# Optimization experiments

Measured on AMD Instinct MI355X. Metric: run time of the kernel, lower is better.

The kernel has to match this reference:

```python
import jax, jax.numpy as jnp
import numpy as np
from jax import lax

DT = 0.01        # self.dt
DT_SCALE = 1.0   # forward default


def _christoffel(v, x, U, W):
    # Low-rank quadratic Christoffel contraction (U, W as in verlet_fused):
    # gamma = (tanh(x @ U) * (v @ U)^2) @ W        [B, D]
    h = v @ U                 # [B, R]
    gate = jnp.tanh(x @ U)    # [B, R]
    return (gate * h * h) @ W


def setup_inputs() -> dict:
    key = jax.random.key(0)
    ks = jax.random.split(key, 5)
    B, D, R = 4096, 1024, 256
    x = jax.random.normal(ks[0], (B, D), dtype=jnp.float32)
    v = jax.random.normal(ks[1], (B, D), dtype=jnp.float32)
    force = jax.random.normal(ks[2], (B, D), dtype=jnp.float32)
    U = jax.random.normal(ks[3], (D, R), dtype=jnp.float32) * (D ** -0.5)
    W = jax.random.normal(ks[4], (R, D), dtype=jnp.float32) * (R ** -0.5)
    return {"x": x, "v": v, "force": force, "U": U, "W": W, "steps": 8}


def reference(x, v, force, U, W, steps):
    dt = jnp.float32(DT * DT_SCALE)
    half = jnp.float32(0.5)

    def step(carry, _):
        x, v = carry
        a = force - _christoffel(v, x, U, W)
        v_half = v + half * dt * a
        x = x + dt * v_half
        a_next = force - _christoffel(v_half, x, U, W)
        v = v_half + half * dt * a_next
        return (x, v), None

    (x, v), _ = lax.scan(step, (x, v), None, length=steps)
    return (x, v)
```

## Files before the change

### kernel.cpp

```cpp
#include <hip/hip_runtime.h>

typedef __bf16 bf16_t;
typedef __bf16 bf16x2 __attribute__((ext_vector_type(2)));
typedef __bf16 bf16x8 __attribute__((ext_vector_type(8)));
typedef float f32x4 __attribute__((ext_vector_type(4)));

#define MFMA_BF16(a, b, c) __builtin_amdgcn_mfma_f32_16x16x32_bf16((a), (b), (c), 0, 0, 0)

static constexpr int Bn = 4096;
static constexpr int Dn = 1024;
static constexpr int Rn = 256;
static constexpr int BT = 16;
static constexpr float DTv = 0.01f;
static constexpr float HDT = 0.005f;

__device__ __forceinline__ int swz(int col) { return col ^ (((col >> 5) & 7) << 2); }

__global__ __launch_bounds__(1024)
void setup_kernel(const float* __restrict__ U, const float* __restrict__ W,
                  bf16_t* __restrict__ Upk, bf16_t* __restrict__ Wpk,
                  bf16_t* __restrict__ WUpk) {
  __shared__ __align__(16) bf16_t wbuf[16 * 1032];
  const int tid = (int)threadIdx.x;
  const int b = (int)blockIdx.x;
  if (b < 32) {
    int t = b * 1024 + tid;
    int l = t & 63, f = t >> 6;
    int kb = f & 31, ct = f >> 5;
    int row0 = kb * 32 + (l >> 4) * 8, col = ct * 16 + (l & 15);
    bf16x8 v;
#pragma unroll
    for (int j = 0; j < 8; ++j) v[j] = (bf16_t)U[(size_t)(row0 + j) * Rn + col];
    ((bf16x8*)Upk)[t] = v;
  } else if (b < 64) {
    int t = (b - 32) * 1024 + tid;
    int l = t & 63, f = t >> 6;
    int kb = f & 7, ct = f >> 3;
    int row0 = kb * 32 + (l >> 4) * 8, col = ct * 16 + (l & 15);
    bf16x8 v;
#pragma unroll
    for (int j = 0; j < 8; ++j) v[j] = (bf16_t)W[(size_t)(row0 + j) * Dn + col];
    ((bf16x8*)Wpk)[t] = v;
  } else {
    const int m = b - 64;
    const int wv = tid >> 6;
    const int l = tid & 63;
    const int ln = l & 15;
    const int quad = l >> 4;
    {
      int row = tid >> 6;
      int c0 = (tid & 63) * 16;
      const float* src = W + (size_t)(m * 16 + row) * Dn + c0;
      bf16_t* dst = wbuf + row * 1032 + c0;
#pragma unroll
      for (int j = 0; j < 16; ++j) dst[j] = (bf16_t)src[j];
    }
    __syncthreads();
    const int ucol = wv * 16 + ln;
    float uf[8][8];
#pragma unroll
    for (int p = 0; p < 8; ++p)
#pragma unroll
      for (int j = 0; j < 8; ++j)
        uf[p][j] = U[(size_t)(p * 32 + quad * 8 + j) * Rn + ucol];
    f32x4 acc = {0.f, 0.f, 0.f, 0.f};
    const bf16_t* arow = wbuf + ln * 1032 + quad * 8;
#pragma unroll
    for (int kb = 0; kb < 32; ++kb) {
      bf16x8 bb;
#pragma unroll
      for (int j = 0; j < 8; ++j) bb[j] = (bf16_t)uf[kb & 7][j];
      const bf16x8 a = *(const bf16x8*)(arow + kb * 32);
      acc = MFMA_BF16(a, bb, acc);
      if (kb < 24) {
#pragma unroll
        for (int j = 0; j < 8; ++j)
          uf[kb & 7][j] = U[(size_t)((kb + 8) * 32 + quad * 8 + j) * Rn + ucol];
      }
    }
#pragma unroll
    for (int r = 0; r < 4; ++r) {
      int rw = m * 16 + quad * 4 + r;
      int kb = rw >> 5;
      int sub = (rw >> 3) & 3;
      int j = rw & 7;
      size_t slot = ((size_t)(wv * 8 + kb) * 64 + sub * 16 + ln) * 8 + j;
      WUpk[slot] = (bf16_t)acc[r];
    }
  }
}

__global__ __launch_bounds__(1024)
__attribute__((amdgpu_waves_per_eu(4, 4)))
void integrate_kernel(const float* __restrict__ x_in, const float* __restrict__ v_in,
                      const float* __restrict__ force,
                      const bf16_t* __restrict__ Upk, const bf16_t* __restrict__ Wpk,
                      const bf16_t* __restrict__ WUpk,
                      const int* __restrict__ steps_p, float* __restrict__ out) {
  __shared__ __align__(16) char smem[99072];
  bf16_t* abuf = (bf16_t*)smem;
  float* fsb = (float*)smem;

  const int tid = (int)threadIdx.x;
  const int wv = tid >> 6;
  const int l = tid & 63;
  const int ln = l & 15;
  const int quad = l >> 4;
  const int s = steps_p[0];
  const int nhalf = 2 * s;
  const int row_base = (int)blockIdx.x * BT;

  float* out_x = out;
  float* out_v = out + (size_t)Bn * Dn;

  float xs[4][4], vs[4][4];
  bf16x2 fs2[4][2];

#pragma unroll
  for (int i = 0; i < 4; ++i) {
    const int col = (wv * 4 + i) * 16 + ln;
#pragma unroll
    for (int r = 0; r < 4; ++r) {
      const size_t g = (size_t)(row_base + quad * 4 + r) * Dn + col;
      xs[i][r] = x_in[g];
      vs[i][r] = v_in[g];
      fs2[i][r >> 1][r & 1] = (bf16_t)force[g];
    }
  }
#pragma unroll
  for (int i = 0; i < 4; ++i) {
    const int col = (wv * 4 + i) * 16 + ln;
#pragma unroll
    for (int r = 0; r < 4; ++r) {
      const int ro = (quad * 4 + r) * 1032 + col;
      abuf[ro] = (bf16_t)xs[i][r];
      abuf[16512 + ro] = (bf16_t)vs[i][r];
      abuf[33024 + ro] = fs2[i][r >> 1][r & 1];
    }
  }
  __syncthreads();

  f32x4 hx = {0.f, 0.f, 0.f, 0.f};
  f32x4 hv = {0.f, 0.f, 0.f, 0.f};
  f32x4 FU = {0.f, 0.f, 0.f, 0.f};
  {
    const bf16x8* up = (const bf16x8*)Upk + (size_t)wv * 32 * 64 + l;
    const bf16_t* ax = abuf + ln * 1032 + quad * 8;
    bf16x8 ur[8];
#pragma unroll
    for (int p = 0; p < 8; ++p) ur[p] = up[p * 64];
#pragma unroll
    for (int kb = 0; kb < 32; ++kb) {
      const bf16x8 b = ur[kb & 7];
      if (kb < 24) ur[kb & 7] = up[(kb + 8) * 64];
      const bf16x8 a0 = *(const bf16x8*)(ax + kb * 32);
      const bf16x8 a1 = *(const bf16x8*)(ax + 16512 + kb * 32);
      const bf16x8 a2 = *(const bf16x8*)(ax + 33024 + kb * 32);
      hx = MFMA_BF16(a0, b, hx);
      hv = MFMA_BF16(a1, b, hv);
      FU = MFMA_BF16(a2, b, FU);
    }
  }
  __syncthreads();

  bf16x8 wu[8];
  {
    const bf16x8* wub = (const bf16x8*)WUpk + (size_t)wv * 8 * 64 + l;
#pragma unroll
    for (int kb = 0; kb < 8; ++kb) wu[kb] = wub[kb * 64];
  }

  f32x4 S1 = {0.f, 0.f, 0.f, 0.f};
  f32x4 S2 = {0.f, 0.f, 0.f, 0.f};
  bf16_t* tbase = (bf16_t*)smem;
  for (int h = 0; h < nhalf; ++h) {
    if (h & 1) {
#pragma unroll
      for (int r = 0; r < 4; ++r) hx[r] += DTv * hv[r];
    }
    const float ch = (float)(s - ((h + 1) >> 1));
    bf16_t* tb = tbase + (h & 1) * 4224;
#pragma unroll
    for (int r = 0; r < 4; ++r) {
      float a = fminf(fmaxf(hx[r], -15.f), 15.f);
      const float e = __expf(2.f * a);
      const float gate = 1.f - 2.f * __builtin_amdgcn_rcpf(e + 1.f);
      const float t = gate * hv[r] * hv[r];
      S1[r] += t;
      S2[r] += ch * t;
      tb[(quad * 4 + r) * 264 + wv * 16 + ln] = (bf16_t)t;
    }
    __syncthreads();
    f32x4 g0 = {0.f, 0.f, 0.f, 0.f};
    f32x4 g1 = {0.f, 0.f, 0.f, 0.f};
    f32x4 g2 = {0.f, 0.f, 0.f, 0.f};
    f32x4 g3 = {0.f, 0.f, 0.f, 0.f};
    const bf16_t* trow = tb + ln * 264 + quad * 8;
    g0 = MFMA_BF16(*(const bf16x8*)(trow + 0 * 32), wu[0], g0);
    g1 = MFMA_BF16(*(const bf16x8*)(trow + 1 * 32), wu[1], g1);
    g2 = MFMA_BF16(*(const bf16x8*)(trow + 2 * 32), wu[2], g2);
    g3 = MFMA_BF16(*(const bf16x8*)(trow + 3 * 32), wu[3], g3);
    g0 = MFMA_BF16(*(const bf16x8*)(trow + 4 * 32), wu[4], g0);
    g1 = MFMA_BF16(*(const bf16x8*)(trow + 5 * 32), wu[5], g1);
    g2 = MFMA_BF16(*(const bf16x8*)(trow + 6 * 32), wu[6], g2);
    g3 = MFMA_BF16(*(const bf16x8*)(trow + 7 * 32), wu[7], g3);
#pragma unroll
    for (int r = 0; r < 4; ++r)
      hv[r] += HDT * (FU[r] - ((g0[r] + g1[r]) + (g2[r] + g3[r])));
  }
  __syncthreads();

  bf16_t* sbuf = (bf16_t*)smem;
#pragma unroll
  for (int r = 0; r < 4; ++r) {
    const int ro = (quad * 4 + r) * 264 + wv * 16 + ln;
    sbuf[ro] = (bf16_t)S1[r];
    sbuf[4224 + ro] = (bf16_t)S2[r];
  }
  __syncthreads();
  f32x4 ac1[4], ac2[4];
#pragma unroll
  for (int i = 0; i < 4; ++i) {
    ac1[i] = (f32x4){0.f, 0.f, 0.f, 0.f};
    ac2[i] = (f32x4){0.f, 0.f, 0.f, 0.f};
  }
  {
    const bf16x8* wp = (const bf16x8*)Wpk + (size_t)(wv * 4) * 8 * 64 + l;
    const bf16_t* s1row = sbuf + ln * 264 + quad * 8;
    const bf16_t* s2row = s1row + 4224;
    bf16x8 wr[4][2];
#pragma unroll
    for (int i = 0; i < 4; ++i) {
      wr[i][0] = wp[i * 512];
      wr[i][1] = wp[i * 512 + 64];
    }
#pragma unroll
    for (int kb = 0; kb < 8; ++kb) {
      const bf16x8 a1 = *(const bf16x8*)(s1row + kb * 32);
      const bf16x8 a2 = *(const bf16x8*)(s2row + kb * 32);
#pragma unroll
      for (int i = 0; i < 4; ++i) {
        const bf16x8 b = wr[i][kb & 1];
        if (kb < 6) wr[i][kb & 1] = wp[i * 512 + (kb + 2) * 64];
        ac1[i] = MFMA_BF16(a1, b, ac1[i]);
        ac2[i] = MFMA_BF16(a2, b, ac2[i]);
      }
    }
  }
  __syncthreads();

  const float sf = (float)s;
  const float c_vf = sf * DTv;
  const float c_xf = sf * sf * DTv * HDT;
  int csw[4];
#pragma unroll
  for (int i = 0; i < 4; ++i) csw[i] = swz((wv * 4 + i) * 16 + ln);
  auto store_chunk = [&](float* __restrict__ dstA, int HF, auto vex) {
    if ((quad >> 1) == HF) {
#pragma unroll
      for (int i = 0; i < 4; ++i)
#pragma unroll
        for (int r = 0; r < 4; ++r)
          fsb[((quad & 1) * 4 + r) * 1024 + csw[i]] = vex(i, r);
    }
    __syncthreads();
    float* dst_ = dstA + (size_t)(row_base + HF * 8) * Dn;
#pragma unroll
    for (int k = 0; k < 2; ++k) {
      const int fi = k * 4096 + tid * 4;
      *(f32x4*)(dst_ + fi) = *(const f32x4*)(fsb + (fi >> 10) * 1024 + swz(fi & 1023));
    }
    __syncthreads();
  };
  auto vval = [&](int i, int r) {
    return vs[i][r] + c_vf * (float)fs2[i][r >> 1][r & 1] - HDT * ac1[i][r];
  };
  auto xval = [&](int i, int r) {
    return xs[i][r] + c_vf * vs[i][r] + c_xf * (float)fs2[i][r >> 1][r & 1] -
           DTv * HDT * ac2[i][r];
  };
  store_chunk(out_v, 0, vval);
  store_chunk(out_v, 1, vval);
  store_chunk(out_x, 0, xval);
  store_chunk(out_x, 1, xval);
}

extern "C" void kernel_launch(void* const* d_in, const int* in_sizes, int n_in,
                              void* d_out, int out_size, void* d_ws, size_t ws_size,
                              hipStream_t stream) {
  const float* x = (const float*)d_in[0];
  const float* v = (const float*)d_in[1];
  const float* force = (const float*)d_in[2];
  const float* U = (const float*)d_in[3];
  const float* W = (const float*)d_in[4];
  const int* steps = (const int*)d_in[5];

  bf16_t* Upk = (bf16_t*)d_ws;
  bf16_t* Wpk = (bf16_t*)((char*)d_ws + 512 * 1024);
  bf16_t* WUpk = (bf16_t*)((char*)d_ws + 1024 * 1024);

  setup_kernel<<<80, 1024, 0, stream>>>(U, W, Upk, Wpk, WUpk);
  integrate_kernel<<<Bn / BT, 1024, 0, stream>>>(x, v, force, Upk, Wpk, WUpk, steps,
                                                 (float*)d_out);
}
```

Baseline: 161.8 us.

## Halve integrate block to 512 threads with two column tiles per wave; coalesce setup packing

The integrate kernel now runs 8 waves per block instead of 16. Each wave owns two R-column tiles and eight D-column tiles, so the A-fragments it reads from LDS feed twice as many MFMAs, and the occupancy hint drops to 2 waves per EU. The setup kernel stages U and W rows through shared memory with vectorized float4 loads before packing them into the MFMA layout, which cuts its block count from 80 to 56. The trade is more registers per thread and fewer waves available to hide latency in the per-step loop.

```diff
diff --git a/kernel.cpp b/kernel.cpp
--- a/kernel.cpp
+++ b/kernel.cpp
@@ -1,7 +1,6 @@
 #include <hip/hip_runtime.h>
 
 typedef __bf16 bf16_t;
-typedef __bf16 bf16x2 __attribute__((ext_vector_type(2)));
 typedef __bf16 bf16x8 __attribute__((ext_vector_type(8)));
 typedef float f32x4 __attribute__((ext_vector_type(4)));
 
@@ -20,33 +19,52 @@
 void setup_kernel(const float* __restrict__ U, const float* __restrict__ W,
                   bf16_t* __restrict__ Upk, bf16_t* __restrict__ Wpk,
                   bf16_t* __restrict__ WUpk) {
-  __shared__ __align__(16) bf16_t wbuf[16 * 1032];
+  __shared__ __align__(16) char ssm[66816];
   const int tid = (int)threadIdx.x;
   const int b = (int)blockIdx.x;
+  const int l = tid & 63;
+  const int wv = tid >> 6;
+  const int ln = l & 15;
+  const int quad = l >> 4;
+
   if (b < 32) {
-    int t = b * 1024 + tid;
-    int l = t & 63, f = t >> 6;
-    int kb = f & 31, ct = f >> 5;
-    int row0 = kb * 32 + (l >> 4) * 8, col = ct * 16 + (l & 15);
+    bf16_t* ubuf = (bf16_t*)ssm;
+    const int row = tid >> 5, c0 = (tid & 31) * 8;
+    const float* src = U + (size_t)(b * 32 + row) * Rn + c0;
+    f32x4 u0 = *(const f32x4*)src;
+    f32x4 u1 = *(const f32x4*)(src + 4);
+    bf16_t* d = ubuf + row * 268 + c0;
+#pragma unroll
+    for (int j = 0; j < 4; ++j) { d[j] = (bf16_t)u0[j]; d[4 + j] = (bf16_t)u1[j]; }
+    __syncthreads();
     bf16x8 v;
 #pragma unroll
-    for (int j = 0; j < 8; ++j) v[j] = (bf16_t)U[(size_t)(row0 + j) * Rn + col];
-    ((bf16x8*)Upk)[t] = v;
-  } else if (b < 64) {
-    int t = (b - 32) * 1024 + tid;
-    int l = t & 63, f = t >> 6;
-    int kb = f & 7, ct = f >> 3;
-    int row0 = kb * 32 + (l >> 4) * 8, col = ct * 16 + (l & 15);
-    bf16x8 v;
-#pragma unroll
-    for (int j = 0; j < 8; ++j) v[j] = (bf16_t)W[(size_t)(row0 + j) * Dn + col];
-    ((bf16x8*)Wpk)[t] = v;
+    for (int j = 0; j < 8; ++j) v[j] = ubuf[(quad * 8 + j) * 268 + wv * 16 + ln];
+    ((bf16x8*)Upk)[(size_t)(wv * 32 + b) * 64 + l] = v;
+  } else if (b < 40) {
+    const int kb = b - 32;
+    bf16_t* wbuf2 = (bf16_t*)ssm;
+    const int row = tid >> 5, c0 = (tid & 31) * 32;
+    const float* src = W + (size_t)(kb * 32 + row) * Dn + c0;
+    bf16_t* d = wbuf2 + row * 1044 + c0;
+#pragma unroll
+    for (int k = 0; k < 8; ++k) {
+      f32x4 u = *(const f32x4*)(src + k * 4);
+#pragma unroll
+      for (int j = 0; j < 4; ++j) d[k * 4 + j] = (bf16_t)u[j];
+    }
+    __syncthreads();
+#pragma unroll
+    for (int cc = 0; cc < 4; ++cc) {
+      const int ct = wv + cc * 16;
+      bf16x8 v;
+#pragma unroll
+      for (int j = 0; j < 8; ++j) v[j] = wbuf2[(quad * 8 + j) * 1044 + ct * 16 + ln];
+      ((bf16x8*)Wpk)[(size_t)(ct * 8 + kb) * 64 + l] = v;
+    }
   } else {
-    const int m = b - 64;
-    const int wv = tid >> 6;
-    const int l = tid & 63;
-    const int ln = l & 15;
-    const int quad = l >> 4;
+    const int m = b - 40;
+    bf16_t* wbuf = (bf16_t*)ssm;
     {
       int row = tid >> 6;
       int c0 = (tid & 63) * 16;
@@ -90,8 +108,8 @@
   }
 }
 
-__global__ __launch_bounds__(1024)
-__attribute__((amdgpu_waves_per_eu(4, 4)))
+__global__ __launch_bounds__(512)
+__attribute__((amdgpu_waves_per_eu(2, 2)))
 void integrate_kernel(const float* __restrict__ x_in, const float* __restrict__ v_in,
                       const float* __restrict__ force,
                       const bf16_t* __restrict__ Upk, const bf16_t* __restrict__ Wpk,
@@ -113,124 +131,144 @@
   float* out_x = out;
   float* out_v = out + (size_t)Bn * Dn;
 
-  float xs[4][4], vs[4][4];
-  bf16x2 fs2[4][2];
-
-#pragma unroll
-  for (int i = 0; i < 4; ++i) {
-    const int col = (wv * 4 + i) * 16 + ln;
+  float xs[8][4], vs[8][4];
+  bf16_t fsv[8][4];
+
+#pragma unroll
+  for (int i = 0; i < 8; ++i) {
+    const int col = (wv * 8 + i) * 16 + ln;
 #pragma unroll
     for (int r = 0; r < 4; ++r) {
       const size_t g = (size_t)(row_base + quad * 4 + r) * Dn + col;
       xs[i][r] = x_in[g];
       vs[i][r] = v_in[g];
-      fs2[i][r >> 1][r & 1] = (bf16_t)force[g];
-    }
-  }
-#pragma unroll
-  for (int i = 0; i < 4; ++i) {
-    const int col = (wv * 4 + i) * 16 + ln;
+      fsv[i][r] = (bf16_t)force[g];
+    }
+  }
+#pragma unroll
+  for (int i = 0; i < 8; ++i) {
+    const int col = (wv * 8 + i) * 16 + ln;
 #pragma unroll
     for (int r = 0; r < 4; ++r) {
       const int ro = (quad * 4 + r) * 1032 + col;
       abuf[ro] = (bf16_t)xs[i][r];
       abuf[16512 + ro] = (bf16_t)vs[i][r];
-      abuf[33024 + ro] = fs2[i][r >> 1][r & 1];
-    }
-  }
-  __syncthreads();
-
-  f32x4 hx = {0.f, 0.f, 0.f, 0.f};
-  f32x4 hv = {0.f, 0.f, 0.f, 0.f};
-  f32x4 FU = {0.f, 0.f, 0.f, 0.f};
+      abuf[33024 + ro] = fsv[i][r];
+    }
+  }
+  __syncthreads();
+
+  f32x4 hx[2], hv[2], FU[2];
+#pragma unroll
+  for (int c = 0; c < 2; ++c) {
+    hx[c] = (f32x4){0.f, 0.f, 0.f, 0.f};
+    hv[c] = (f32x4){0.f, 0.f, 0.f, 0.f};
+    FU[c] = (f32x4){0.f, 0.f, 0.f, 0.f};
+  }
   {
-    const bf16x8* up = (const bf16x8*)Upk + (size_t)wv * 32 * 64 + l;
+    const bf16x8* up = (const bf16x8*)Upk + (size_t)(wv * 64) * 64 + l;
     const bf16_t* ax = abuf + ln * 1032 + quad * 8;
     bf16x8 ur[8];
 #pragma unroll
     for (int p = 0; p < 8; ++p) ur[p] = up[p * 64];
 #pragma unroll
-    for (int kb = 0; kb < 32; ++kb) {
-      const bf16x8 b = ur[kb & 7];
-      if (kb < 24) ur[kb & 7] = up[(kb + 8) * 64];
+    for (int f = 0; f < 64; ++f) {
+      const bf16x8 bfr = ur[f & 7];
+      if (f < 56) ur[f & 7] = up[(f + 8) * 64];
+      const int kb = f & 31, c = f >> 5;
       const bf16x8 a0 = *(const bf16x8*)(ax + kb * 32);
       const bf16x8 a1 = *(const bf16x8*)(ax + 16512 + kb * 32);
       const bf16x8 a2 = *(const bf16x8*)(ax + 33024 + kb * 32);
-      hx = MFMA_BF16(a0, b, hx);
-      hv = MFMA_BF16(a1, b, hv);
-      FU = MFMA_BF16(a2, b, FU);
-    }
-  }
-  __syncthreads();
-
-  bf16x8 wu[8];
+      hx[c] = MFMA_BF16(a0, bfr, hx[c]);
+      hv[c] = MFMA_BF16(a1, bfr, hv[c]);
+      FU[c] = MFMA_BF16(a2, bfr, FU[c]);
+    }
+  }
+  __syncthreads();
+
+  bf16x8 wu[2][8];
   {
-    const bf16x8* wub = (const bf16x8*)WUpk + (size_t)wv * 8 * 64 + l;
-#pragma unroll
-    for (int kb = 0; kb < 8; ++kb) wu[kb] = wub[kb * 64];
-  }
-
-  f32x4 S1 = {0.f, 0.f, 0.f, 0.f};
-  f32x4 S2 = {0.f, 0.f, 0.f, 0.f};
+    const bf16x8* wub = (const bf16x8*)WUpk + (size_t)(wv * 2) * 8 * 64 + l;
+#pragma unroll
+    for (int c = 0; c < 2; ++c)
+#pragma unroll
+      for (int kb = 0; kb < 8; ++kb) wu[c][kb] = wub[(c * 8 + kb) * 64];
+  }
+
+  f32x4 S1[2], S2[2];
+#pragma unroll
+  for (int c = 0; c < 2; ++c) {
+    S1[c] = (f32x4){0.f, 0.f, 0.f, 0.f};
+    S2[c] = (f32x4){0.f, 0.f, 0.f, 0.f};
+  }
   bf16_t* tbase = (bf16_t*)smem;
   for (int h = 0; h < nhalf; ++h) {
     if (h & 1) {
 #pragma unroll
-      for (int r = 0; r < 4; ++r) hx[r] += DTv * hv[r];
+      for (int c = 0; c < 2; ++c)
+#pragma unroll
+        for (int r = 0; r < 4; ++r) hx[c][r] += DTv * hv[c][r];
     }
     const float ch = (float)(s - ((h + 1) >> 1));
     bf16_t* tb = tbase + (h & 1) * 4224;
 #pragma unroll
+    for (int c = 0; c < 2; ++c)
+#pragma unroll
+      for (int r = 0; r < 4; ++r) {
+        float a = fminf(fmaxf(hx[c][r], -15.f), 15.f);
+        const float e = __expf(2.f * a);
+        const float gate = 1.f - 2.f * __builtin_amdgcn_rcpf(e + 1.f);
+        const float t = gate * hv[c][r] * hv[c][r];
+        S1[c][r] += t;
+        S2[c][r] += ch * t;
+        tb[(quad * 4 + r) * 264 + (wv * 2 + c) * 16 + ln] = (bf16_t)t;
+      }
+    __syncthreads();
+    const bf16_t* trow = tb + ln * 264 + quad * 8;
+    bf16x8 a[8];
+#pragma unroll
+    for (int kb = 0; kb < 8; ++kb) a[kb] = *(const bf16x8*)(trow + kb * 32);
+    f32x4 g[2][2];
+#pragma unroll
+    for (int c = 0; c < 2; ++c)
+#pragma unroll
+      for (int p = 0; p < 2; ++p) g[c][p] = (f32x4){0.f, 0.f, 0.f, 0.f};
+#pragma unroll
+    for (int kb = 0; kb < 8; ++kb) {
+      g[0][kb & 1] = MFMA_BF16(a[kb], wu[0][kb], g[0][kb & 1]);
+      g[1][kb & 1] = MFMA_BF16(a[kb], wu[1][kb], g[1][kb & 1]);
+    }
+#pragma unroll
+    for (int c = 0; c < 2; ++c)
+#pragma unroll
+      for (int r = 0; r < 4; ++r)
+        hv[c][r] += HDT * (FU[c][r] - (g[c][0][r] + g[c][1][r]));
+  }
+  __syncthreads();
+
+  bf16_t* sbuf = (bf16_t*)smem;
+#pragma unroll
+  for (int c = 0; c < 2; ++c)
+#pragma unroll
     for (int r = 0; r < 4; ++r) {
-      float a = fminf(fmaxf(hx[r], -15.f), 15.f);
-      const float e = __expf(2.f * a);
-      const float gate = 1.f - 2.f * __builtin_amdgcn_rcpf(e + 1.f);
-      const float t = gate * hv[r] * hv[r];
-      S1[r] += t;
-      S2[r] += ch * t;
-      tb[(quad * 4 + r) * 264 + wv * 16 + ln] = (bf16_t)t;
-    }
-    __syncthreads();
-    f32x4 g0 = {0.f, 0.f, 0.f, 0.f};
-    f32x4 g1 = {0.f, 0.f, 0.f, 0.f};
-    f32x4 g2 = {0.f, 0.f, 0.f, 0.f};
-    f32x4 g3 = {0.f, 0.f, 0.f, 0.f};
-    const bf16_t* trow = tb + ln * 264 + quad * 8;
-    g0 = MFMA_BF16(*(const bf16x8*)(trow + 0 * 32), wu[0], g0);
-    g1 = MFMA_BF16(*(const bf16x8*)(trow + 1 * 32), wu[1], g1);
-    g2 = MFMA_BF16(*(const bf16x8*)(trow + 2 * 32), wu[2], g2);
-    g3 = MFMA_BF16(*(const bf16x8*)(trow + 3 * 32), wu[3], g3);
-    g0 = MFMA_BF16(*(const bf16x8*)(trow + 4 * 32), wu[4], g0);
-    g1 = MFMA_BF16(*(const bf16x8*)(trow + 5 * 32), wu[5], g1);
-    g2 = MFMA_BF16(*(const bf16x8*)(trow + 6 * 32), wu[6], g2);
-    g3 = MFMA_BF16(*(const bf16x8*)(trow + 7 * 32), wu[7], g3);
-#pragma unroll
-    for (int r = 0; r < 4; ++r)
-      hv[r] += HDT * (FU[r] - ((g0[r] + g1[r]) + (g2[r] + g3[r])));
-  }
-  __syncthreads();
-
-  bf16_t* sbuf = (bf16_t*)smem;
-#pragma unroll
-  for (int r = 0; r < 4; ++r) {
-    const int ro = (quad * 4 + r) * 264 + wv * 16 + ln;
-    sbuf[ro] = (bf16_t)S1[r];
-    sbuf[4224 + ro] = (bf16_t)S2[r];
-  }
-  __syncthreads();
-  f32x4 ac1[4], ac2[4];
-#pragma unroll
-  for (int i = 0; i < 4; ++i) {
+      const int ro = (quad * 4 + r) * 264 + (wv * 2 + c) * 16 + ln;
+      sbuf[ro] = (bf16_t)S1[c][r];
+      sbuf[4224 + ro] = (bf16_t)S2[c][r];
+    }
+  __syncthreads();
+  f32x4 ac1[8], ac2[8];
+#pragma unroll
+  for (int i = 0; i < 8; ++i) {
     ac1[i] = (f32x4){0.f, 0.f, 0.f, 0.f};
     ac2[i] = (f32x4){0.f, 0.f, 0.f, 0.f};
   }
   {
-    const bf16x8* wp = (const bf16x8*)Wpk + (size_t)(wv * 4) * 8 * 64 + l;
+    const bf16x8* wp = (const bf16x8*)Wpk + (size_t)(wv * 8) * 8 * 64 + l;
     const bf16_t* s1row = sbuf + ln * 264 + quad * 8;
     const bf16_t* s2row = s1row + 4224;
-    bf16x8 wr[4][2];
-#pragma unroll
-    for (int i = 0; i < 4; ++i) {
+    bf16x8 wr[8][2];
+#pragma unroll
+    for (int i = 0; i < 8; ++i) {
       wr[i][0] = wp[i * 512];
       wr[i][1] = wp[i * 512 + 64];
     }
@@ -239,11 +277,11 @@
       const bf16x8 a1 = *(const bf16x8*)(s1row + kb * 32);
       const bf16x8 a2 = *(const bf16x8*)(s2row + kb * 32);
 #pragma unroll
-      for (int i = 0; i < 4; ++i) {
-        const bf16x8 b = wr[i][kb & 1];
+      for (int i = 0; i < 8; ++i) {
+        const bf16x8 bfr = wr[i][kb & 1];
         if (kb < 6) wr[i][kb & 1] = wp[i * 512 + (kb + 2) * 64];
-        ac1[i] = MFMA_BF16(a1, b, ac1[i]);
-        ac2[i] = MFMA_BF16(a2, b, ac2[i]);
+        ac1[i] = MFMA_BF16(a1, bfr, ac1[i]);
+        ac2[i] = MFMA_BF16(a2, bfr, ac2[i]);
       }
     }
   }
@@ -252,13 +290,13 @@
   const float sf = (float)s;
   const float c_vf = sf * DTv;
   const float c_xf = sf * sf * DTv * HDT;
-  int csw[4];
-#pragma unroll
-  for (int i = 0; i < 4; ++i) csw[i] = swz((wv * 4 + i) * 16 + ln);
+  int csw[8];
+#pragma unroll
+  for (int i = 0; i < 8; ++i) csw[i] = swz((wv * 8 + i) * 16 + ln);
   auto store_chunk = [&](float* __restrict__ dstA, int HF, auto vex) {
     if ((quad >> 1) == HF) {
 #pragma unroll
-      for (int i = 0; i < 4; ++i)
+      for (int i = 0; i < 8; ++i)
 #pragma unroll
         for (int r = 0; r < 4; ++r)
           fsb[((quad & 1) * 4 + r) * 1024 + csw[i]] = vex(i, r);
@@ -266,18 +304,17 @@
     __syncthreads();
     float* dst_ = dstA + (size_t)(row_base + HF * 8) * Dn;
 #pragma unroll
-    for (int k = 0; k < 2; ++k) {
-      const int fi = k * 4096 + tid * 4;
+    for (int k = 0; k < 4; ++k) {
+      const int fi = k * 2048 + tid * 4;
       *(f32x4*)(dst_ + fi) = *(const f32x4*)(fsb + (fi >> 10) * 1024 + swz(fi & 1023));
     }
     __syncthreads();
   };
   auto vval = [&](int i, int r) {
-    return vs[i][r] + c_vf * (float)fs2[i][r >> 1][r & 1] - HDT * ac1[i][r];
+    return vs[i][r] + c_vf * (float)fsv[i][r] - HDT * ac1[i][r];
   };
   auto xval = [&](int i, int r) {
-    return xs[i][r] + c_vf * vs[i][r] + c_xf * (float)fs2[i][r >> 1][r & 1] -
-           DTv * HDT * ac2[i][r];
+    return xs[i][r] + c_vf * vs[i][r] + c_xf * (float)fsv[i][r] - DTv * HDT * ac2[i][r];
   };
   store_chunk(out_v, 0, vval);
   store_chunk(out_v, 1, vval);
@@ -299,7 +336,7 @@
   bf16_t* Wpk = (bf16_t*)((char*)d_ws + 512 * 1024);
   bf16_t* WUpk = (bf16_t*)((char*)d_ws + 1024 * 1024);
 
-  setup_kernel<<<80, 1024, 0, stream>>>(U, W, Upk, Wpk, WUpk);
-  integrate_kernel<<<Bn / BT, 1024, 0, stream>>>(x, v, force, Upk, Wpk, WUpk, steps,
-                                                 (float*)d_out);
+  setup_kernel<<<56, 1024, 0, stream>>>(U, W, Upk, Wpk, WUpk);
+  integrate_kernel<<<Bn / BT, 512, 0, stream>>>(x, v, force, Upk, Wpk, WUpk, steps,
+                                                (float*)d_out);
 }
```

New measurement: 169.5 us. +4.8%, slower.

## Fuse weight-packing setup into integrate kernel with cooperative grid sync

Applied to the files above, without the earlier changes.

Merges the separate setup kernel (packing U, W and W·U to bf16) into the integration kernel, launched cooperatively with a grid-wide barrier after the per-block x/v/force staging. The first 56 blocks do the packing work, now with coalesced vector loads staged through LDS, before joining the integration. This removes one kernel launch and the gap between the two kernels. In exchange it adds a grid sync, requires all 256 blocks to be co-resident, and puts the packing work on the critical path of a few blocks.

```diff
diff --git a/kernel.cpp b/kernel.cpp
--- a/kernel.cpp
+++ b/kernel.cpp
@@ -1,7 +1,7 @@
 #include <hip/hip_runtime.h>
+#include <hip/hip_cooperative_groups.h>
 
 typedef __bf16 bf16_t;
-typedef __bf16 bf16x2 __attribute__((ext_vector_type(2)));
 typedef __bf16 bf16x8 __attribute__((ext_vector_type(8)));
 typedef float f32x4 __attribute__((ext_vector_type(4)));
 
@@ -17,36 +17,70 @@
 __device__ __forceinline__ int swz(int col) { return col ^ (((col >> 5) & 7) << 2); }
 
 __global__ __launch_bounds__(1024)
-void setup_kernel(const float* __restrict__ U, const float* __restrict__ W,
+__attribute__((amdgpu_waves_per_eu(4, 4)))
+void fused_kernel(const float* __restrict__ x_in, const float* __restrict__ v_in,
+                  const float* __restrict__ force,
+                  const float* __restrict__ U, const float* __restrict__ W,
                   bf16_t* __restrict__ Upk, bf16_t* __restrict__ Wpk,
-                  bf16_t* __restrict__ WUpk) {
-  __shared__ __align__(16) bf16_t wbuf[16 * 1032];
+                  bf16_t* __restrict__ WUpk,
+                  const int* __restrict__ steps_p, float* __restrict__ out) {
+  __shared__ __align__(16) char smem[99072];
+  bf16_t* abuf = (bf16_t*)smem;
+  float* fsb = (float*)smem;
+
   const int tid = (int)threadIdx.x;
   const int b = (int)blockIdx.x;
+  const int wv = tid >> 6;
+  const int l = tid & 63;
+  const int ln = l & 15;
+  const int quad = l >> 4;
+  const int s = steps_p[0];
+  const int nhalf = 2 * s;
+  const int row_base = b * BT;
+
+  float* out_x = out;
+  float* out_v = out + (size_t)Bn * Dn;
+
   if (b < 32) {
-    int t = b * 1024 + tid;
-    int l = t & 63, f = t >> 6;
-    int kb = f & 31, ct = f >> 5;
-    int row0 = kb * 32 + (l >> 4) * 8, col = ct * 16 + (l & 15);
+    bf16_t* ubuf = (bf16_t*)smem;
+    const int row = tid >> 5, c0 = (tid & 31) * 8;
+    const float* src = U + (size_t)(b * 32 + row) * Rn + c0;
+    f32x4 u0 = *(const f32x4*)src;
+    f32x4 u1 = *(const f32x4*)(src + 4);
+    bf16_t* d = ubuf + row * 268 + c0;
+#pragma unroll
+    for (int j = 0; j < 4; ++j) { d[j] = (bf16_t)u0[j]; d[4 + j] = (bf16_t)u1[j]; }
+    __syncthreads();
     bf16x8 v;
 #pragma unroll
-    for (int j = 0; j < 8; ++j) v[j] = (bf16_t)U[(size_t)(row0 + j) * Rn + col];
-    ((bf16x8*)Upk)[t] = v;
-  } else if (b < 64) {
-    int t = (b - 32) * 1024 + tid;
-    int l = t & 63, f = t >> 6;
-    int kb = f & 7, ct = f >> 3;
-    int row0 = kb * 32 + (l >> 4) * 8, col = ct * 16 + (l & 15);
-    bf16x8 v;
-#pragma unroll
-    for (int j = 0; j < 8; ++j) v[j] = (bf16_t)W[(size_t)(row0 + j) * Dn + col];
-    ((bf16x8*)Wpk)[t] = v;
-  } else {
-    const int m = b - 64;
-    const int wv = tid >> 6;
-    const int l = tid & 63;
-    const int ln = l & 15;
-    const int quad = l >> 4;
+    for (int j = 0; j < 8; ++j) v[j] = ubuf[(quad * 8 + j) * 268 + wv * 16 + ln];
+    ((bf16x8*)Upk)[(size_t)(wv * 32 + b) * 64 + l] = v;
+    __syncthreads();
+  } else if (b < 40) {
+    const int kb = b - 32;
+    bf16_t* wbuf2 = (bf16_t*)smem;
+    const int row = tid >> 5, c0 = (tid & 31) * 32;
+    const float* src = W + (size_t)(kb * 32 + row) * Dn + c0;
+    bf16_t* d = wbuf2 + row * 1044 + c0;
+#pragma unroll
+    for (int k = 0; k < 8; ++k) {
+      f32x4 u = *(const f32x4*)(src + k * 4);
+#pragma unroll
+      for (int j = 0; j < 4; ++j) d[k * 4 + j] = (bf16_t)u[j];
+    }
+    __syncthreads();
+#pragma unroll
+    for (int cc = 0; cc < 4; ++cc) {
+      const int ct = wv + cc * 16;
+      bf16x8 v;
+#pragma unroll
+      for (int j = 0; j < 8; ++j) v[j] = wbuf2[(quad * 8 + j) * 1044 + ct * 16 + ln];
+      ((bf16x8*)Wpk)[(size_t)(ct * 8 + kb) * 64 + l] = v;
+    }
+    __syncthreads();
+  } else if (b < 56) {
+    const int m = b - 40;
+    bf16_t* wbuf = (bf16_t*)smem;
     {
       int row = tid >> 6;
       int c0 = (tid & 63) * 16;
@@ -87,34 +121,11 @@
       size_t slot = ((size_t)(wv * 8 + kb) * 64 + sub * 16 + ln) * 8 + j;
       WUpk[slot] = (bf16_t)acc[r];
     }
-  }
-}
-
-__global__ __launch_bounds__(1024)
-__attribute__((amdgpu_waves_per_eu(4, 4)))
-void integrate_kernel(const float* __restrict__ x_in, const float* __restrict__ v_in,
-                      const float* __restrict__ force,
-                      const bf16_t* __restrict__ Upk, const bf16_t* __restrict__ Wpk,
-                      const bf16_t* __restrict__ WUpk,
-                      const int* __restrict__ steps_p, float* __restrict__ out) {
-  __shared__ __align__(16) char smem[99072];
-  bf16_t* abuf = (bf16_t*)smem;
-  float* fsb = (float*)smem;
-
-  const int tid = (int)threadIdx.x;
-  const int wv = tid >> 6;
-  const int l = tid & 63;
-  const int ln = l & 15;
-  const int quad = l >> 4;
-  const int s = steps_p[0];
-  const int nhalf = 2 * s;
-  const int row_base = (int)blockIdx.x * BT;
-
-  float* out_x = out;
-  float* out_v = out + (size_t)Bn * Dn;
+    __syncthreads();
+  }
 
   float xs[4][4], vs[4][4];
-  bf16x2 fs2[4][2];
+  bf16_t fsv[4][4];
 
 #pragma unroll
   for (int i = 0; i < 4; ++i) {
@@ -124,7 +135,7 @@
       const size_t g = (size_t)(row_base + quad * 4 + r) * Dn + col;
       xs[i][r] = x_in[g];
       vs[i][r] = v_in[g];
-      fs2[i][r >> 1][r & 1] = (bf16_t)force[g];
+      fsv[i][r] = (bf16_t)force[g];
     }
   }
 #pragma unroll
@@ -135,10 +146,19 @@
       const int ro = (quad * 4 + r) * 1032 + col;
       abuf[ro] = (bf16_t)xs[i][r];
       abuf[16512 + ro] = (bf16_t)vs[i][r];
-      abuf[33024 + ro] = fs2[i][r >> 1][r & 1];
-    }
-  }
-  __syncthreads();
+      abuf[33024 + ro] = fsv[i][r];
+    }
+  }
+  __threadfence();
+
+  cooperative_groups::this_grid().sync();
+
+  bf16x8 wu[8];
+  {
+    const bf16x8* wub = (const bf16x8*)WUpk + (size_t)wv * 8 * 64 + l;
+#pragma unroll
+    for (int kb = 0; kb < 8; ++kb) wu[kb] = wub[kb * 64];
+  }
 
   f32x4 hx = {0.f, 0.f, 0.f, 0.f};
   f32x4 hv = {0.f, 0.f, 0.f, 0.f};
@@ -151,24 +171,17 @@
     for (int p = 0; p < 8; ++p) ur[p] = up[p * 64];
 #pragma unroll
     for (int kb = 0; kb < 32; ++kb) {
-      const bf16x8 b = ur[kb & 7];
+      const bf16x8 bb = ur[kb & 7];
       if (kb < 24) ur[kb & 7] = up[(kb + 8) * 64];
       const bf16x8 a0 = *(const bf16x8*)(ax + kb * 32);
       const bf16x8 a1 = *(const bf16x8*)(ax + 16512 + kb * 32);
       const bf16x8 a2 = *(const bf16x8*)(ax + 33024 + kb * 32);
-      hx = MFMA_BF16(a0, b, hx);
-      hv = MFMA_BF16(a1, b, hv);
-      FU = MFMA_BF16(a2, b, FU);
+      hx = MFMA_BF16(a0, bb, hx);
+      hv = MFMA_BF16(a1, bb, hv);
+      FU = MFMA_BF16(a2, bb, FU);
     }
   }
   __syncthreads();
-
-  bf16x8 wu[8];
-  {
-    const bf16x8* wub = (const bf16x8*)WUpk + (size_t)wv * 8 * 64 + l;
-#pragma unroll
-    for (int kb = 0; kb < 8; ++kb) wu[kb] = wub[kb * 64];
-  }
 
   f32x4 S1 = {0.f, 0.f, 0.f, 0.f};
   f32x4 S2 = {0.f, 0.f, 0.f, 0.f};
@@ -240,10 +253,10 @@
       const bf16x8 a2 = *(const bf16x8*)(s2row + kb * 32);
 #pragma unroll
       for (int i = 0; i < 4; ++i) {
-        const bf16x8 b = wr[i][kb & 1];
+        const bf16x8 bb = wr[i][kb & 1];
         if (kb < 6) wr[i][kb & 1] = wp[i * 512 + (kb + 2) * 64];
-        ac1[i] = MFMA_BF16(a1, b, ac1[i]);
-        ac2[i] = MFMA_BF16(a2, b, ac2[i]);
+        ac1[i] = MFMA_BF16(a1, bb, ac1[i]);
+        ac2[i] = MFMA_BF16(a2, bb, ac2[i]);
       }
     }
   }
@@ -273,11 +286,10 @@
     __syncthreads();
   };
   auto vval = [&](int i, int r) {
-    return vs[i][r] + c_vf * (float)fs2[i][r >> 1][r & 1] - HDT * ac1[i][r];
+    return vs[i][r] + c_vf * (float)fsv[i][r] - HDT * ac1[i][r];
   };
   auto xval = [&](int i, int r) {
-    return xs[i][r] + c_vf * vs[i][r] + c_xf * (float)fs2[i][r >> 1][r & 1] -
-           DTv * HDT * ac2[i][r];
+    return xs[i][r] + c_vf * vs[i][r] + c_xf * (float)fsv[i][r] - DTv * HDT * ac2[i][r];
   };
   store_chunk(out_v, 0, vval);
   store_chunk(out_v, 1, vval);
@@ -298,8 +310,10 @@
   bf16_t* Upk = (bf16_t*)d_ws;
   bf16_t* Wpk = (bf16_t*)((char*)d_ws + 512 * 1024);
   bf16_t* WUpk = (bf16_t*)((char*)d_ws + 1024 * 1024);
-
-  setup_kernel<<<80, 1024, 0, stream>>>(U, W, Upk, Wpk, WUpk);
-  integrate_kernel<<<Bn / BT, 1024, 0, stream>>>(x, v, force, Upk, Wpk, WUpk, steps,
-                                                 (float*)d_out);
+  float* out_f = (float*)d_out;
+
+  void* args[] = {(void*)&x, (void*)&v, (void*)&force, (void*)&U, (void*)&W,
+                  (void*)&Upk, (void*)&Wpk, (void*)&WUpk, (void*)&steps, (void*)&out_f};
+  hipLaunchCooperativeKernel((const void*)fused_kernel, dim3(Bn / BT), dim3(1024), args,
+                             0, stream);
 }
```

Measured after the change: 369.5 us. 128% more time.
